# Kernel optimization log

Measured on AMD Instinct MI355X. Metric: run time of the kernel, lower is better.

## Reference

```python
import jax, jax.numpy as jnp
import numpy as np

N_NODES = 100000


def gcn_conv(x, src, dst, w, b, num_nodes):
    """PyG-style GCNConv with self-loops and symmetric normalization.

    x: [N, Fin], src/dst: [E'] int (already include self loops), w: [Fin, Fout], b: [Fout]
    """
    h = x @ w  # [N, Fout]
    deg = jax.ops.segment_sum(jnp.ones_like(dst, dtype=h.dtype), dst, num_segments=num_nodes)
    dinv = jnp.where(deg > 0, jax.lax.rsqrt(jnp.maximum(deg, 1.0)), 0.0)
    norm = dinv[src] * dinv[dst]  # [E']
    msg = h[src] * norm[:, None]  # [E', Fout] -- dominant memory traffic
    out = jax.ops.segment_sum(msg, dst, num_segments=num_nodes)  # scatter-add into targets
    return out + b


def setup_inputs() -> dict:
    key = jax.random.key(0)
    k1, k2, k3, k4, k5, k6 = jax.random.split(key, 6)
    N, E, Fin, Fout = N_NODES, 3200000, 128, 64
    hid = 2 * Fout  # 128
    x = jax.random.normal(k1, (N, Fin), dtype=jnp.float32)
    edge_index = jax.random.randint(k2, (2, E), 0, N, dtype=jnp.int64)
    # glorot-ish scale for weights
    w1 = jax.random.normal(k3, (Fin, hid), dtype=jnp.float32) * np.sqrt(2.0 / (Fin + hid))
    b1 = jax.random.normal(k4, (hid,), dtype=jnp.float32) * 0.01
    w2 = jax.random.normal(k5, (hid, Fout), dtype=jnp.float32) * np.sqrt(2.0 / (hid + Fout))
    b2 = jax.random.normal(k6, (Fout,), dtype=jnp.float32) * 0.01
    return {"x": x, "edge_index": edge_index, "w1": w1, "b1": b1, "w2": w2, "b2": b2}


def reference(x, edge_index, w1, b1, w2, b2):
    N = x.shape[0]
    loops = jnp.arange(N, dtype=edge_index.dtype)
    src = jnp.concatenate([edge_index[0], loops])
    dst = jnp.concatenate([edge_index[1], loops])
    h = jax.nn.relu(gcn_conv(x, src, dst, w1, b1, N))
    out = gcn_conv(h, src, dst, w2, b2, N)
    return out
```

## Files before the change

### kernel.cpp

```cpp
#include <hip/hip_runtime.h>
#include <hip/hip_fp16.h>
#include <type_traits>


constexpr int B = 1024;
constexpr int KB = 256;

using half8 = __attribute__((ext_vector_type(8))) _Float16;
using f32x4 = __attribute__((ext_vector_type(4))) float;

__global__ void detect_i64(const int* __restrict__ idx32, int* __restrict__ flag) {
    int v = idx32[2 * threadIdx.x + 1];
    unsigned long long b = __ballot(v != 0);
    if (threadIdx.x == 0) flag[0] = (b == 0ULL) ? 1 : 0;
}

__device__ __forceinline__ int load_idx(const void* edges, size_t i, int is64) {
    return is64 ? (int)((const long long*)edges)[i] : ((const int*)edges)[i];
}

__device__ __forceinline__ int clampN(int v, int N) {
    return ((unsigned)v < (unsigned)N) ? v : 0;
}

__global__ __launch_bounds__(1024) void bucket_count(
    const void* __restrict__ edges, int E, int EPB, int NR,
    const int* __restrict__ flag, int* __restrict__ cnt, int N) {
    __shared__ int hist[B];
    int t = threadIdx.x, b = blockIdx.x;
    for (int k = t; k < B; k += 1024) hist[k] = 0;
    __syncthreads();
    int is64 = flag[0];
    int start = b * EPB, end = min(E, start + EPB);
    int j = start + t;
    for (; j + 3 * 1024 < end; j += 4 * 1024) {
        int d[4];
#pragma unroll
        for (int u = 0; u < 4; ++u)
            d[u] = clampN(load_idx(edges, (size_t)E + j + u * 1024, is64), N) / NR;
#pragma unroll
        for (int u = 0; u < 4; ++u) atomicAdd(&hist[d[u]], 1);
    }
    for (; j < end; j += 1024) {
        int d = clampN(load_idx(edges, (size_t)E + j, is64), N);
        atomicAdd(&hist[d / NR], 1);
    }
    __syncthreads();
    for (int k = t; k < B; k += 1024) cnt[(size_t)k * KB + b] = hist[k];
}

__global__ void scan_partials(const int* __restrict__ in, int* __restrict__ partials, int M) {
    __shared__ int sm[256];
    int t = threadIdx.x, i = blockIdx.x * 256 + t;
    sm[t] = (i < M) ? in[i] : 0;
    __syncthreads();
    for (int off = 128; off > 0; off >>= 1) {
        if (t < off) sm[t] += sm[t + off];
        __syncthreads();
    }
    if (t == 0) partials[blockIdx.x] = sm[0];
}

__global__ void scan_scan(int* __restrict__ partials, int NB) {
    __shared__ int sm[1024];
    int t = threadIdx.x;
    int v = (t < NB) ? partials[t] : 0;
    sm[t] = v; __syncthreads();
    for (int off = 1; off < 1024; off <<= 1) {
        int x = sm[t];
        int y = (t >= off) ? sm[t - off] : 0;
        __syncthreads();
        sm[t] = x + y;
        __syncthreads();
    }
    if (t < NB) partials[t] = (t == 0) ? 0 : sm[t - 1];
}

__global__ void scan_write(const int* __restrict__ in, const int* __restrict__ partials,
                           int* __restrict__ out, int M) {
    __shared__ int sm[256];
    int t = threadIdx.x, b = blockIdx.x, i = b * 256 + t;
    int v = (i < M) ? in[i] : 0;
    sm[t] = v; __syncthreads();
    for (int off = 1; off < 256; off <<= 1) {
        int x = sm[t];
        int y = (t >= off) ? sm[t - off] : 0;
        __syncthreads();
        sm[t] = x + y;
        __syncthreads();
    }
    if (i < M) out[i] = partials[b] + sm[t] - v;
}

__global__ __launch_bounds__(1024) void bucket_scatter(
    const void* __restrict__ edges, int E, int EPB, int NR,
    const int* __restrict__ flag, const int* __restrict__ base,
    int* __restrict__ buck, int N) {
    __shared__ int cur[B];
    int t = threadIdx.x, b = blockIdx.x;
    for (int k = t; k < B; k += 1024) cur[k] = base[(size_t)k * KB + b];
    __syncthreads();
    int is64 = flag[0];
    int start = b * EPB, end = min(E, start + EPB);
    int j = start + t;
    for (; j + 3 * 1024 < end; j += 4 * 1024) {
        int s[4], bin[4], dl[4], pos[4];
#pragma unroll
        for (int u = 0; u < 4; ++u) {
            int jj = j + u * 1024;
            s[u] = clampN(load_idx(edges, (size_t)jj, is64), N);
            int d = clampN(load_idx(edges, (size_t)E + jj, is64), N);
            bin[u] = d / NR;
            dl[u] = d - bin[u] * NR;
        }
#pragma unroll
        for (int u = 0; u < 4; ++u) pos[u] = atomicAdd(&cur[bin[u]], 1);
#pragma unroll
        for (int u = 0; u < 4; ++u) buck[pos[u]] = (dl[u] << 17) | s[u];
    }
    for (; j < end; j += 1024) {
        int s = clampN(load_idx(edges, (size_t)j, is64), N);
        int d = clampN(load_idx(edges, (size_t)E + j, is64), N);
        int bin = d / NR;
        int dl = d - bin * NR;
        int pos = atomicAdd(&cur[bin], 1);
        buck[pos] = (dl << 17) | s;
    }
}

__global__ __launch_bounds__(256) void bucket_csr(
    const int* __restrict__ buck, const int* __restrict__ base, int E, int NR,
    float* __restrict__ dinv, int* __restrict__ rowptr,
    int* __restrict__ colx, int N) {
    __shared__ int hist[128];
    __shared__ int cnt0[128];
    __shared__ int cur[128];
    int t = threadIdx.x, b = blockIdx.x;
    if (b == 0 && t == 0) rowptr[N] = E;
    int d0 = b * NR;
    if (d0 >= N) return;
    int nr = min(NR, N - d0);
    int segbase = base[(size_t)b * KB];
    int segend = (b == B - 1) ? E : base[(size_t)(b + 1) * KB];

    if (t < 128) hist[t] = 0;
    __syncthreads();
    {
        int j = segbase + t;
        for (; j + 3 * 256 < segend; j += 4 * 256) {
            int v[4];
#pragma unroll
            for (int u = 0; u < 4; ++u) v[u] = buck[j + u * 256] >> 17;
#pragma unroll
            for (int u = 0; u < 4; ++u) atomicAdd(&hist[v[u]], 1);
        }
        for (; j < segend; j += 256) atomicAdd(&hist[buck[j] >> 17], 1);
    }
    __syncthreads();
    if (t < 128) cnt0[t] = hist[t];
    __syncthreads();
    for (int off = 1; off < 128; off <<= 1) {
        int v = 0;
        if (t < 128 && t >= off) v = hist[t - off];
        __syncthreads();
        if (t < 128) hist[t] += v;
        __syncthreads();
    }
    if (t < 128) {
        int ex = hist[t] - cnt0[t];
        cur[t] = ex;
        if (t < nr) {
            rowptr[d0 + t] = segbase + ex;
            dinv[d0 + t] = rsqrtf((float)(cnt0[t] + 1));
        }
    }
    __syncthreads();
    {
        int j = segbase + t;
        for (; j + 3 * 256 < segend; j += 4 * 256) {
            int v[4], pos[4];
#pragma unroll
            for (int u = 0; u < 4; ++u) v[u] = buck[j + u * 256];
#pragma unroll
            for (int u = 0; u < 4; ++u) pos[u] = atomicAdd(&cur[v[u] >> 17], 1);
#pragma unroll
            for (int u = 0; u < 4; ++u) colx[segbase + pos[u]] = v[u] & 0x1FFFF;
        }
        for (; j < segend; j += 256) {
            int v = buck[j];
            int pos = segbase + atomicAdd(&cur[v >> 17], 1);
            colx[pos] = v & 0x1FFFF;
        }
    }
}

template <typename XT>
__global__ __launch_bounds__(256) void gemm_mfma(
    const XT* __restrict__ X, const float* __restrict__ W,
    const float* __restrict__ dinv, __half* __restrict__ G, int M, int Ncols) {
    constexpr int BK = 128;
    constexpr int LDP = BK + 8;
    __shared__ _Float16 xA[64][LDP];
    __shared__ _Float16 wB[64][LDP];
    const int t = threadIdx.x;
    const int m0 = blockIdx.x * 64;
    const int c0 = blockIdx.y * 64;

    {
        int r = t & 63, kg = t >> 6;
        int row = m0 + r; if (row >= M) row = M - 1;
        const XT* xr = &X[(size_t)row * BK + kg * 32];
        if constexpr (std::is_same<XT, __half>::value) {
            const uint4* src = (const uint4*)xr;
            uint4* dst = (uint4*)&xA[r][kg * 32];
#pragma unroll
            for (int q = 0; q < 4; ++q) dst[q] = src[q];
        } else {
#pragma unroll
            for (int c = 0; c < 32; c += 8) {
                float4 a = *(const float4*)&xr[c];
                float4 b = *(const float4*)&xr[c + 4];
                half8 h;
                h[0] = (_Float16)a.x; h[1] = (_Float16)a.y;
                h[2] = (_Float16)a.z; h[3] = (_Float16)a.w;
                h[4] = (_Float16)b.x; h[5] = (_Float16)b.y;
                h[6] = (_Float16)b.z; h[7] = (_Float16)b.w;
                *(half8*)&xA[r][kg * 32 + c] = h;
            }
        }
    }
    {
        int cg = t & 15, k0 = t >> 4;
#pragma unroll
        for (int kk = 0; kk < 8; ++kk) {
            int k = k0 + kk * 16;
            float4 wv = *(const float4*)&W[(size_t)k * Ncols + c0 + cg * 4];
            wB[cg * 4 + 0][k] = (_Float16)wv.x;
            wB[cg * 4 + 1][k] = (_Float16)wv.y;
            wB[cg * 4 + 2][k] = (_Float16)wv.z;
            wB[cg * 4 + 3][k] = (_Float16)wv.w;
        }
    }
    __syncthreads();

    const int wv = t >> 6;
    const int lane = t & 63;
    const int fr = lane & 15;
    const int kg8 = (lane >> 4) * 8;
    f32x4 acc0 = {0.f, 0.f, 0.f, 0.f};
    f32x4 acc1 = {0.f, 0.f, 0.f, 0.f};
    f32x4 acc2 = {0.f, 0.f, 0.f, 0.f};
    f32x4 acc3 = {0.f, 0.f, 0.f, 0.f};

#pragma unroll
    for (int ks = 0; ks < BK; ks += 32) {
        half8 af = *(half8*)&xA[wv * 16 + fr][ks + kg8];
        half8 b0 = *(half8*)&wB[0 * 16 + fr][ks + kg8];
        half8 b1 = *(half8*)&wB[1 * 16 + fr][ks + kg8];
        half8 b2 = *(half8*)&wB[2 * 16 + fr][ks + kg8];
        half8 b3 = *(half8*)&wB[3 * 16 + fr][ks + kg8];
        acc0 = __builtin_amdgcn_mfma_f32_16x16x32_f16(af, b0, acc0, 0, 0, 0);
        acc1 = __builtin_amdgcn_mfma_f32_16x16x32_f16(af, b1, acc1, 0, 0, 0);
        acc2 = __builtin_amdgcn_mfma_f32_16x16x32_f16(af, b2, acc2, 0, 0, 0);
        acc3 = __builtin_amdgcn_mfma_f32_16x16x32_f16(af, b3, acc3, 0, 0, 0);
    }

    int r0 = wv * 16 + (lane >> 4) * 4;
    float dv[4];
    bool ok[4];
#pragma unroll
    for (int i = 0; i < 4; ++i) {
        int row = m0 + r0 + i;
        ok[i] = row < M;
        dv[i] = ok[i] ? dinv[row] : 0.f;
    }
    const f32x4* accs[4] = {&acc0, &acc1, &acc2, &acc3};
#pragma unroll
    for (int fc = 0; fc < 4; ++fc) {
        int col = c0 + fc * 16 + fr;
#pragma unroll
        for (int i = 0; i < 4; ++i) {
            if (ok[i]) {
                int row = m0 + r0 + i;
                G[(size_t)row * Ncols + col] = __float2half((*accs[fc])[i] * dv[i]);
            }
        }
    }
}

__global__ __launch_bounds__(256) void agg_split(
    const __half* __restrict__ G, const int* __restrict__ rowptr,
    const int* __restrict__ colx, const float* __restrict__ dinv,
    const float* __restrict__ bias, __half* __restrict__ Out, int N, int p) {
    constexpr int UNR = 16;
    int wid = (int)((blockIdx.x * 256 + threadIdx.x) >> 6);
    int lane = threadIdx.x & 63;
    if (wid >= N) return;
    int s = rowptr[wid], e = rowptr[wid + 1];
    int emain = s + ((e - s) & ~(UNR - 1));

    const unsigned* gp = (const unsigned*)G;
    int dw = p * 32 + (lane & 31);
    int half = lane >> 5;

    __half2 z = __floats2half2_rn(0.f, 0.f);
    unsigned su = gp[(size_t)wid * 64 + dw];
    __half2 hacc = half ? z : *(__half2*)&su;
    __half2 hacc2 = z;

    for (int j = s; j < emain; j += UNR) {
        int cl = colx[j + (lane & 15)];
        unsigned v[UNR / 2];
#pragma unroll
        for (int u = 0; u < UNR; u += 2) {
            int c0 = __builtin_amdgcn_readlane(cl, u);
            int c1 = __builtin_amdgcn_readlane(cl, u + 1);
            int cu = half ? c1 : c0;
            v[u / 2] = gp[(size_t)cu * 64 + dw];
        }
#pragma unroll
        for (int u = 0; u < UNR; u += 4) {
            hacc  = __hadd2(hacc,  *(__half2*)&v[u / 2]);
            hacc2 = __hadd2(hacc2, *(__half2*)&v[u / 2 + 1]);
        }
    }
    if (emain < e) {
        int cl = clampN(colx[min(emain + (lane & 15), e - 1)], N);
        const __half2 one2 = __floats2half2_rn(1.f, 1.f);
#pragma unroll
        for (int u = 0; u < UNR; u += 2) {
            int c0 = __builtin_amdgcn_readlane(cl, u);
            int c1 = __builtin_amdgcn_readlane(cl, u + 1);
            int cu = half ? c1 : c0;
            unsigned vv = gp[(size_t)cu * 64 + dw];
            int jj = emain + u + half;
            __half2 w = (jj < e) ? one2 : z;
            hacc = __hfma2(w, *(__half2*)&vv, hacc);
        }
    }

    hacc = __hadd2(hacc, hacc2);
    int bits = *(int*)&hacc;
    int other = __shfl_xor(bits, 32, 64);
    __half2 ho = *(__half2*)&other;
    float2 f1 = __half22float2(hacc);
    float2 f2 = __half22float2(ho);
    float ax = f1.x + f2.x, ay = f1.y + f2.y;

    if (half == 0) {
        float d = dinv[wid];
        float2 bv = *(const float2*)&bias[dw * 2];
        float ox = fmaf(d, ax, bv.x);
        float oy = fmaf(d, ay, bv.y);
        ox = fmaxf(ox, 0.f); oy = fmaxf(oy, 0.f);
        __half2 h = __floats2half2_rn(ox, oy);
        ((unsigned*)Out)[(size_t)wid * 64 + dw] = *(unsigned*)&h;
    }
}

template <int UNR>
__global__ __launch_bounds__(256) void agg2_kernel(
    const __half* __restrict__ G, const int* __restrict__ rowptr,
    const int* __restrict__ colx, const float* __restrict__ dinv,
    const float* __restrict__ bias, float* __restrict__ Out, int N) {
    static_assert(UNR == 16, "readlane batch hard-coded to 16");
    int wid = (int)((blockIdx.x * 256 + threadIdx.x) >> 6);
    int lane = threadIdx.x & 63;
    if (wid >= N) return;
    int s = rowptr[wid], e = rowptr[wid + 1];
    int emain = s + ((e - s) & ~(UNR - 1));

    const unsigned* gp = (const unsigned*)G;
    const int dw = lane & 31;

    unsigned su = gp[((size_t)wid << 5) + dw];
    __half2 hacc = *(__half2*)&su;
    __half2 hacc2 = __floats2half2_rn(0.f, 0.f);

    for (int j = s; j < emain; j += UNR) {
        int cl = colx[j + (lane & 15)];
        unsigned v[UNR];
#pragma unroll
        for (int u = 0; u < UNR; ++u) {
            int cu = __builtin_amdgcn_readlane(cl, u);
            v[u] = gp[((size_t)cu << 5) + dw];
        }
#pragma unroll
        for (int u = 0; u < UNR; u += 2) {
            hacc  = __hadd2(hacc,  *(__half2*)&v[u]);
            hacc2 = __hadd2(hacc2, *(__half2*)&v[u + 1]);
        }
    }
    if (emain < e) {
        int cl = clampN(colx[min(emain + (lane & 15), e - 1)], N);
        const __half2 one2 = __floats2half2_rn(1.f, 1.f);
        const __half2 zero2 = __floats2half2_rn(0.f, 0.f);
#pragma unroll
        for (int u = 0; u < UNR; ++u) {
            int cu = __builtin_amdgcn_readlane(cl, u);
            unsigned vv = gp[((size_t)cu << 5) + dw];
            __half2 w = (emain + u < e) ? one2 : zero2;
            hacc = __hfma2(w, *(__half2*)&vv, hacc);
        }
    }

    float2 f1 = __half22float2(hacc);
    float2 f2 = __half22float2(hacc2);
    float ax = f1.x + f2.x, ay = f1.y + f2.y;
    float d = dinv[wid];
    if (lane < 32) {
        float2 bv = *(const float2*)&bias[dw * 2];
        float2 o;
        o.x = fmaf(d, ax, bv.x);
        o.y = fmaf(d, ay, bv.y);
        *(float2*)&Out[(size_t)wid * 64 + dw * 2] = o;
    }
}

extern "C" void kernel_launch(void* const* d_in, const int* in_sizes, int n_in,
                              void* d_out, int out_size, void* d_ws, size_t ws_size,
                              hipStream_t stream) {
    const float* x  = (const float*)d_in[0];
    const void*  ei = d_in[1];
    const float* w1 = (const float*)d_in[2];
    const float* b1 = (const float*)d_in[3];
    const float* w2 = (const float*)d_in[4];
    const float* b2 = (const float*)d_in[5];
    float* out = (float*)d_out;

    const int N  = in_sizes[0] / 128;
    const int E  = in_sizes[1] / 2;
    const int M  = B * KB;
    const int NR = (N + B - 1) / B;

    char* p = (char*)d_ws;
    auto carve = [&](size_t bytes) {
        void* r = (void*)p;
        p += (bytes + 255) & ~(size_t)255;
        return r;
    };
    int*    cnt      = (int*)carve((size_t)M * 4);
    int*    base     = (int*)carve((size_t)M * 4);
    int*    partials = (int*)carve(1024 * 4);
    int*    flag     = (int*)carve(256);
    int*    rowptr   = (int*)carve((size_t)(N + 1) * 4);
    float*  dinv     = (float*)carve((size_t)N * 4);
    int*    colx     = (int*)carve((size_t)E * 4);
    __half* g1       = (__half*)carve((size_t)N * 128 * 2);
    __half* a1       = (__half*)carve((size_t)N * 128 * 2);
    __half* g2       = g1;
    int*    buck     = (int*)a1;

    const int EPB = (E + KB - 1) / KB;
    const int NBS = M / 256;

    detect_i64<<<1, 64, 0, stream>>>((const int*)ei, flag);
    bucket_count<<<KB, 1024, 0, stream>>>(ei, E, EPB, NR, flag, cnt, N);
    scan_partials<<<NBS, 256, 0, stream>>>(cnt, partials, M);
    scan_scan<<<1, 1024, 0, stream>>>(partials, NBS);
    scan_write<<<NBS, 256, 0, stream>>>(cnt, partials, base, M);
    bucket_scatter<<<KB, 1024, 0, stream>>>(ei, E, EPB, NR, flag, base, buck, N);
    bucket_csr<<<B, 256, 0, stream>>>(buck, base, E, NR, dinv, rowptr, colx, N);

    dim3 grid1((N + 63) / 64, 2);
    gemm_mfma<float><<<grid1, 256, 0, stream>>>(x, w1, dinv, g1, N, 128);
    const int aggb = (N + 3) / 4;
    agg_split<<<aggb, 256, 0, stream>>>(g1, rowptr, colx, dinv, b1, a1, N, 0);
    agg_split<<<aggb, 256, 0, stream>>>(g1, rowptr, colx, dinv, b1, a1, N, 1);

    dim3 grid2((N + 63) / 64, 1);
    gemm_mfma<__half><<<grid2, 256, 0, stream>>>(a1, w2, dinv, g2, N, 64);
    agg2_kernel<16><<<aggb, 256, 0, stream>>>(g2, rowptr, colx, dinv, b2, out, N);
}
```

Baseline: 284.4 us.

## Store layer-1 features in 16-column slices and aggregate per slice

The first GEMM now writes its output in a sliced layout of 8 slabs, each holding 16 fp16 columns per node. A new sliced aggregation kernel interleaves slices across blocks, so each slab (about 3.2MB) can stay in cache while it is gathered, with 8 edges per wave at 32 bytes per row. The second GEMM reads the sliced activations, and layer 2 now uses the paired-edge gather kernel instead of the old 16-unrolled one. This trades full-row coalescing for smaller gather footprints, and it adds a shuffle reduction across edge groups.

```diff
diff --git a/kernel.cpp b/kernel.cpp
--- a/kernel.cpp
+++ b/kernel.cpp
@@ -194,7 +194,7 @@
     }
 }
 
-template <typename XT>
+template <typename XT, bool INS, bool OUTS>
 __global__ __launch_bounds__(256) void gemm_mfma(
     const XT* __restrict__ X, const float* __restrict__ W,
     const float* __restrict__ dinv, __half* __restrict__ G, int M, int Ncols) {
@@ -209,13 +209,19 @@
     {
         int r = t & 63, kg = t >> 6;
         int row = m0 + r; if (row >= M) row = M - 1;
-        const XT* xr = &X[(size_t)row * BK + kg * 32];
-        if constexpr (std::is_same<XT, __half>::value) {
-            const uint4* src = (const uint4*)xr;
+        if constexpr (INS) {
+            const uint4* s0 = (const uint4*)&X[((size_t)(2 * kg) * M + row) * 16];
+            const uint4* s1 = (const uint4*)&X[((size_t)(2 * kg + 1) * M + row) * 16];
+            uint4* dst = (uint4*)&xA[r][kg * 32];
+            dst[0] = s0[0]; dst[1] = s0[1];
+            dst[2] = s1[0]; dst[3] = s1[1];
+        } else if constexpr (std::is_same<XT, __half>::value) {
+            const uint4* src = (const uint4*)&X[(size_t)row * BK + kg * 32];
             uint4* dst = (uint4*)&xA[r][kg * 32];
 #pragma unroll
             for (int q = 0; q < 4; ++q) dst[q] = src[q];
         } else {
+            const XT* xr = &X[(size_t)row * BK + kg * 32];
 #pragma unroll
             for (int c = 0; c < 32; c += 8) {
                 float4 a = *(const float4*)&xr[c];
@@ -277,21 +283,84 @@
     const f32x4* accs[4] = {&acc0, &acc1, &acc2, &acc3};
 #pragma unroll
     for (int fc = 0; fc < 4; ++fc) {
-        int col = c0 + fc * 16 + fr;
 #pragma unroll
         for (int i = 0; i < 4; ++i) {
             if (ok[i]) {
                 int row = m0 + r0 + i;
-                G[(size_t)row * Ncols + col] = __float2half((*accs[fc])[i] * dv[i]);
+                __half h = __float2half((*accs[fc])[i] * dv[i]);
+                if constexpr (OUTS) {
+                    int sl = c0 / 16 + fc;
+                    G[((size_t)sl * M + row) * 16 + fr] = h;
+                } else {
+                    G[(size_t)row * Ncols + c0 + fc * 16 + fr] = h;
+                }
             }
         }
     }
 }
 
-__global__ __launch_bounds__(256) void agg_split(
+__global__ __launch_bounds__(256) void agg1_sliced(
     const __half* __restrict__ G, const int* __restrict__ rowptr,
     const int* __restrict__ colx, const float* __restrict__ dinv,
-    const float* __restrict__ bias, __half* __restrict__ Out, int N, int p) {
+    const float* __restrict__ bias, __half* __restrict__ Out, int N) {
+    int sl = blockIdx.x & 7;
+    int nid = (int)((blockIdx.x >> 3) * 4) + (threadIdx.x >> 6);
+    int lane = threadIdx.x & 63;
+    if (nid >= N) return;
+    int e8 = lane >> 3, d8 = lane & 7;
+    int s = rowptr[nid], e = rowptr[nid + 1];
+    int emain = s + ((e - s) & ~7);
+
+    const unsigned* gp = (const unsigned*)G + (size_t)sl * N * 8;
+    __half2 z = __floats2half2_rn(0.f, 0.f);
+    unsigned su = gp[(size_t)nid * 8 + d8];
+    __half2 acc = (e8 == 0) ? *(__half2*)&su : z;
+    __half2 acc2 = z;
+
+    int j = s;
+    for (; j + 8 < emain; j += 16) {
+        int c0i = colx[j + e8];
+        int c1i = colx[j + 8 + e8];
+        unsigned v0 = gp[(size_t)c0i * 8 + d8];
+        unsigned v1 = gp[(size_t)c1i * 8 + d8];
+        acc  = __hadd2(acc,  *(__half2*)&v0);
+        acc2 = __hadd2(acc2, *(__half2*)&v1);
+    }
+    for (; j < emain; j += 8) {
+        int ci = colx[j + e8];
+        unsigned v = gp[(size_t)ci * 8 + d8];
+        acc = __hadd2(acc, *(__half2*)&v);
+    }
+    if (emain < e) {
+        int jj = min(emain + e8, e - 1);
+        int ci = clampN(colx[jj], N);
+        unsigned v = gp[(size_t)ci * 8 + d8];
+        __half2 w = (emain + e8 < e) ? __floats2half2_rn(1.f, 1.f) : z;
+        acc = __hfma2(w, *(__half2*)&v, acc);
+    }
+    acc = __hadd2(acc, acc2);
+#pragma unroll
+    for (int off = 8; off < 64; off <<= 1) {
+        int bits = *(int*)&acc;
+        int ob = __shfl_xor(bits, off, 64);
+        acc = __hadd2(acc, *(__half2*)&ob);
+    }
+    if (e8 == 0) {
+        float2 f = __half22float2(acc);
+        float d = dinv[nid];
+        float2 bv = *(const float2*)&bias[sl * 16 + d8 * 2];
+        float ox = fmaf(d, f.x, bv.x);
+        float oy = fmaf(d, f.y, bv.y);
+        ox = fmaxf(ox, 0.f); oy = fmaxf(oy, 0.f);
+        __half2 h = __floats2half2_rn(ox, oy);
+        ((unsigned*)Out)[(size_t)sl * N * 8 + (size_t)nid * 8 + d8] = *(unsigned*)&h;
+    }
+}
+
+__global__ __launch_bounds__(256) void agg2_pair(
+    const __half* __restrict__ G, const int* __restrict__ rowptr,
+    const int* __restrict__ colx, const float* __restrict__ dinv,
+    const float* __restrict__ bias, float* __restrict__ Out, int N) {
     constexpr int UNR = 16;
     int wid = (int)((blockIdx.x * 256 + threadIdx.x) >> 6);
     int lane = threadIdx.x & 63;
@@ -300,11 +369,11 @@
     int emain = s + ((e - s) & ~(UNR - 1));
 
     const unsigned* gp = (const unsigned*)G;
-    int dw = p * 32 + (lane & 31);
+    int dw = lane & 31;
     int half = lane >> 5;
 
     __half2 z = __floats2half2_rn(0.f, 0.f);
-    unsigned su = gp[(size_t)wid * 64 + dw];
+    unsigned su = gp[(size_t)wid * 32 + dw];
     __half2 hacc = half ? z : *(__half2*)&su;
     __half2 hacc2 = z;
 
@@ -316,7 +385,7 @@
             int c0 = __builtin_amdgcn_readlane(cl, u);
             int c1 = __builtin_amdgcn_readlane(cl, u + 1);
             int cu = half ? c1 : c0;
-            v[u / 2] = gp[(size_t)cu * 64 + dw];
+            v[u / 2] = gp[(size_t)cu * 32 + dw];
         }
 #pragma unroll
         for (int u = 0; u < UNR; u += 4) {
@@ -332,7 +401,7 @@
             int c0 = __builtin_amdgcn_readlane(cl, u);
             int c1 = __builtin_amdgcn_readlane(cl, u + 1);
             int cu = half ? c1 : c0;
-            unsigned vv = gp[(size_t)cu * 64 + dw];
+            unsigned vv = gp[(size_t)cu * 32 + dw];
             int jj = emain + u + half;
             __half2 w = (jj < e) ? one2 : z;
             hacc = __hfma2(w, *(__half2*)&vv, hacc);
@@ -349,66 +418,6 @@
 
     if (half == 0) {
         float d = dinv[wid];
-        float2 bv = *(const float2*)&bias[dw * 2];
-        float ox = fmaf(d, ax, bv.x);
-        float oy = fmaf(d, ay, bv.y);
-        ox = fmaxf(ox, 0.f); oy = fmaxf(oy, 0.f);
-        __half2 h = __floats2half2_rn(ox, oy);
-        ((unsigned*)Out)[(size_t)wid * 64 + dw] = *(unsigned*)&h;
-    }
-}
-
-template <int UNR>
-__global__ __launch_bounds__(256) void agg2_kernel(
-    const __half* __restrict__ G, const int* __restrict__ rowptr,
-    const int* __restrict__ colx, const float* __restrict__ dinv,
-    const float* __restrict__ bias, float* __restrict__ Out, int N) {
-    static_assert(UNR == 16, "readlane batch hard-coded to 16");
-    int wid = (int)((blockIdx.x * 256 + threadIdx.x) >> 6);
-    int lane = threadIdx.x & 63;
-    if (wid >= N) return;
-    int s = rowptr[wid], e = rowptr[wid + 1];
-    int emain = s + ((e - s) & ~(UNR - 1));
-
-    const unsigned* gp = (const unsigned*)G;
-    const int dw = lane & 31;
-
-    unsigned su = gp[((size_t)wid << 5) + dw];
-    __half2 hacc = *(__half2*)&su;
-    __half2 hacc2 = __floats2half2_rn(0.f, 0.f);
-
-    for (int j = s; j < emain; j += UNR) {
-        int cl = colx[j + (lane & 15)];
-        unsigned v[UNR];
-#pragma unroll
-        for (int u = 0; u < UNR; ++u) {
-            int cu = __builtin_amdgcn_readlane(cl, u);
-            v[u] = gp[((size_t)cu << 5) + dw];
-        }
-#pragma unroll
-        for (int u = 0; u < UNR; u += 2) {
-            hacc  = __hadd2(hacc,  *(__half2*)&v[u]);
-            hacc2 = __hadd2(hacc2, *(__half2*)&v[u + 1]);
-        }
-    }
-    if (emain < e) {
-        int cl = clampN(colx[min(emain + (lane & 15), e - 1)], N);
-        const __half2 one2 = __floats2half2_rn(1.f, 1.f);
-        const __half2 zero2 = __floats2half2_rn(0.f, 0.f);
-#pragma unroll
-        for (int u = 0; u < UNR; ++u) {
-            int cu = __builtin_amdgcn_readlane(cl, u);
-            unsigned vv = gp[((size_t)cu << 5) + dw];
-            __half2 w = (emain + u < e) ? one2 : zero2;
-            hacc = __hfma2(w, *(__half2*)&vv, hacc);
-        }
-    }
-
-    float2 f1 = __half22float2(hacc);
-    float2 f2 = __half22float2(hacc2);
-    float ax = f1.x + f2.x, ay = f1.y + f2.y;
-    float d = dinv[wid];
-    if (lane < 32) {
         float2 bv = *(const float2*)&bias[dw * 2];
         float2 o;
         o.x = fmaf(d, ax, bv.x);
@@ -463,12 +472,11 @@
     bucket_csr<<<B, 256, 0, stream>>>(buck, base, E, NR, dinv, rowptr, colx, N);
 
     dim3 grid1((N + 63) / 64, 2);
-    gemm_mfma<float><<<grid1, 256, 0, stream>>>(x, w1, dinv, g1, N, 128);
-    const int aggb = (N + 3) / 4;
-    agg_split<<<aggb, 256, 0, stream>>>(g1, rowptr, colx, dinv, b1, a1, N, 0);
-    agg_split<<<aggb, 256, 0, stream>>>(g1, rowptr, colx, dinv, b1, a1, N, 1);
+    gemm_mfma<float, false, true><<<grid1, 256, 0, stream>>>(x, w1, dinv, g1, N, 128);
+    const int aggb1 = ((N + 3) / 4) * 8;
+    agg1_sliced<<<aggb1, 256, 0, stream>>>(g1, rowptr, colx, dinv, b1, a1, N);
 
     dim3 grid2((N + 63) / 64, 1);
-    gemm_mfma<__half><<<grid2, 256, 0, stream>>>(a1, w2, dinv, g2, N, 64);
-    agg2_kernel<16><<<aggb, 256, 0, stream>>>(g2, rowptr, colx, dinv, b2, out, N);
-}
+    gemm_mfma<__half, true, false><<<grid2, 256, 0, stream>>>(a1, w2, dinv, g2, N, 64);
+    agg2_pair<<<(N + 3) / 4, 256, 0, stream>>>(g2, rowptr, colx, dinv, b2, out, N);
+}
```

After: 420.5 us. +47.8%, slower.
